# Kernel tuning notes

Measured on AMD Instinct MI355X. Metric: run time of the kernel, lower is better.

The kernel has to match this reference:

```python
import jax, jax.numpy as jnp
import numpy as np

N = 16384
IN_FEATS = 256
OUT_FEATS = 256


def setup_inputs() -> dict:
    key = jax.random.key(0)
    k1, k2, k3, k4 = jax.random.split(key, 4)
    # dense (row-normalized-ish) adjacency; scaled so aggregated values stay O(1)
    graph = jax.random.uniform(k1, (N, N), dtype=jnp.float32) / N
    features = jax.random.normal(k2, (N, IN_FEATS), dtype=jnp.float32)
    # nn.Linear params: W [out, in], b [out]
    W = jax.random.normal(k3, (OUT_FEATS, IN_FEATS), dtype=jnp.float32) / np.sqrt(IN_FEATS)
    b = jax.random.normal(k4, (OUT_FEATS,), dtype=jnp.float32) * 0.01
    return {"graph": graph, "features": features, "W": W, "b": b}


def reference(graph, features, W, b):
    # h = graph @ features  (GCN-style dense neighbor aggregation)
    h = jnp.matmul(graph, features)            # [N, in_feats]
    # linear: h @ W.T + b
    h = jnp.einsum('ni,oi->no', h, W) + b      # [N, out_feats]
    # activation = relu (norm = None)
    return jax.nn.relu(h)
```

## Files before the change

kernel.cpp:

```cpp
#include <hip/hip_runtime.h>
#include <hip/hip_bf16.h>

typedef float f32x4 __attribute__((ext_vector_type(4)));
typedef short short8 __attribute__((ext_vector_type(8)));
typedef __bf16 bf16x8 __attribute__((ext_vector_type(8)));

#define N_TOT 16384
#define FEATS 256
#define BM 128
#define BK 32
#define KSPLIT 4
#define NSTEPS ((N_TOT / KSPLIT) / BK)
#define LDSA_BYTES (BM * 128)
#define LDSB_BYTES (FEATS * 64)
#define TILE_BYTES (LDSA_BYTES + LDSB_BYTES)

static __device__ __forceinline__ ushort f2bf(float f) {
  union { __hip_bfloat16 b; ushort u; } cv;
  cv.b = __float2bfloat16(f);
  return cv.u;
}
static __device__ __forceinline__ float bf2f(ushort u) {
  union { unsigned int i; float f; } c;
  c.i = ((unsigned int)u) << 16;
  return c.f;
}
static __device__ __forceinline__ void gload_lds16(const void* g, void* l) {
  __builtin_amdgcn_global_load_lds((const __attribute__((address_space(1))) unsigned int*)g,
                                   (__attribute__((address_space(3))) unsigned int*)l,
                                   16, 0, 0);
}

__global__ __launch_bounds__(256) void k_transpose(const float* __restrict__ feat,
                                                   ushort* __restrict__ fT) {
  __shared__ float tile[64][65];
  const int tx = threadIdx.x & 63, ty = threadIdx.x >> 6;
  const int k0 = blockIdx.x * 64, n0 = blockIdx.y * 64;
#pragma unroll
  for (int j = 0; j < 64; j += 4)
    tile[ty + j][tx] = feat[(size_t)(k0 + ty + j) * FEATS + n0 + tx];
  __syncthreads();
#pragma unroll
  for (int j = 0; j < 64; j += 4)
    fT[(size_t)(n0 + ty + j) * N_TOT + k0 + tx] = f2bf(tile[tx][ty + j]);
}

__global__ __launch_bounds__(256) void k_convw(const float* __restrict__ W,
                                               ushort* __restrict__ Wb) {
  int i = (blockIdx.x * 256 + threadIdx.x) * 4;
  float4 v = *(const float4*)(W + i);
  ushort4 h = { f2bf(v.x), f2bf(v.y), f2bf(v.z), f2bf(v.w) };
  *(ushort4*)(Wb + i) = h;
}

__global__ __launch_bounds__(512, 4) void k_gemm1(const float* __restrict__ graph,
                                                  const ushort* __restrict__ fT,
                                                  ushort* __restrict__ parts) {
  __shared__ char lds[2][TILE_BYTES];
  const int tid = threadIdx.x;
  const int lane = tid & 63, w = tid >> 6;
  const int wm = w >> 2, wn = w & 3;

  const int b = blockIdx.x;
  const int xcd = b & 7;
  const int kb = xcd >> 1;
  const int mi = (b >> 3) | ((xcd & 1) << 6);
  const size_t m0 = (size_t)mi * BM;
  const int kbase = kb * (N_TOT / KSPLIT);
  const int ph = (b * 53) & (NSTEPS - 1);

  auto stage = [&](int bf, int t) {
    const int k0 = kbase + t * BK;
    char* ldsA = &lds[bf][0];
    char* ldsB = &lds[bf][LDSA_BYTES];
#pragma unroll
    for (int j = 0; j < 2; ++j) {
      const int r0 = w * 16 + j * 8;
      const int row = r0 + (lane >> 3);
      const int c = (lane & 7) ^ (row & 7);
      gload_lds16(graph + (m0 + row) * (size_t)N_TOT + k0 + c * 4, ldsA + r0 * 128);
    }
#pragma unroll
    for (int j = 0; j < 2; ++j) {
      const int r0 = w * 32 + j * 16;
      const int row = r0 + (lane >> 2);
      const int c = (lane & 3) ^ (row & 3);
      gload_lds16(fT + (size_t)row * N_TOT + k0 + c * 8, ldsB + r0 * 64);
    }
  };

  f32x4 acc[4][4] = {};
  const int rsel = lane & 15;
  const int kg = lane >> 4;

  auto compute = [&](int bf) {
    const char* Ab = &lds[bf][0];
    const char* Bb = &lds[bf][LDSA_BYTES];
    short8 bfr[4];
#pragma unroll
    for (int nf = 0; nf < 4; ++nf) {
      const int row = wn * 64 + nf * 16 + rsel;
      const int c = kg ^ (row & 3);
      bfr[nf] = *(const short8*)(Bb + row * 64 + c * 16);
    }
#pragma unroll
    for (int mf = 0; mf < 4; ++mf) {
      const int row = wm * 64 + mf * 16 + rsel;
      const int cb = (row & 7);
      const float4 a0 = *(const float4*)(Ab + row * 128 + ((kg * 2) ^ cb) * 16);
      const float4 a1 = *(const float4*)(Ab + row * 128 + ((kg * 2 + 1) ^ cb) * 16);
      short8 af = { (short)f2bf(a0.x), (short)f2bf(a0.y), (short)f2bf(a0.z), (short)f2bf(a0.w),
                    (short)f2bf(a1.x), (short)f2bf(a1.y), (short)f2bf(a1.z), (short)f2bf(a1.w) };
#pragma unroll
      for (int nf = 0; nf < 4; ++nf)
        acc[mf][nf] = __builtin_amdgcn_mfma_f32_16x16x32_bf16(
            __builtin_bit_cast(bf16x8, af), __builtin_bit_cast(bf16x8, bfr[nf]),
            acc[mf][nf], 0, 0, 0);
    }
  };

  stage(0, ph);
  stage(1, (ph + 1) & (NSTEPS - 1));

  for (int s = 0; s < NSTEPS - 2; ++s) {
    asm volatile("s_waitcnt vmcnt(4)" ::: "memory");
    __builtin_amdgcn_s_barrier();
    __builtin_amdgcn_sched_barrier(0);
    compute(s & 1);
    __builtin_amdgcn_s_barrier();
    stage(s & 1, (s + 2 + ph) & (NSTEPS - 1));
  }
  asm volatile("s_waitcnt vmcnt(4)" ::: "memory");
  __builtin_amdgcn_s_barrier();
  __builtin_amdgcn_sched_barrier(0);
  compute((NSTEPS - 2) & 1);
  asm volatile("s_waitcnt vmcnt(0)" ::: "memory");
  __builtin_amdgcn_s_barrier();
  __builtin_amdgcn_sched_barrier(0);
  compute((NSTEPS - 1) & 1);

  ushort* p = parts + (size_t)kb * N_TOT * FEATS;
#pragma unroll
  for (int mf = 0; mf < 4; ++mf)
#pragma unroll
    for (int nf = 0; nf < 4; ++nf)
#pragma unroll
      for (int j = 0; j < 4; ++j) {
        const int row = wm * 64 + mf * 16 + ((lane >> 4) << 2) + j;
        const int col = wn * 64 + nf * 16 + (lane & 15);
        p[(m0 + row) * FEATS + col] = f2bf(acc[mf][nf][j]);
      }
}

__global__ __launch_bounds__(256) void k_gemm2(const ushort* __restrict__ parts,
                                               const ushort* __restrict__ Wb,
                                               const float* __restrict__ bias,
                                               float* __restrict__ out) {
  __shared__ ushort Al[64][264];
  __shared__ ushort Bl[FEATS][40];
  const int tid = threadIdx.x;
  const int lane = tid & 63, w = tid >> 6;
  const size_t m0 = (size_t)blockIdx.x * 64;

  for (int c = tid; c < 2048; c += 256) {
    const int row = c >> 5;
    const int k8 = (c & 31) << 3;
    const size_t off = (m0 + row) * FEATS + k8;
    float s[8] = {0, 0, 0, 0, 0, 0, 0, 0};
#pragma unroll
    for (int p = 0; p < KSPLIT; ++p) {
      const short8 v = *(const short8*)(parts + (size_t)p * N_TOT * FEATS + off);
#pragma unroll
      for (int j = 0; j < 8; ++j) s[j] += bf2f((ushort)v[j]);
    }
    short8 ov;
#pragma unroll
    for (int j = 0; j < 8; ++j) ov[j] = (short)f2bf(s[j]);
    *(short8*)&Al[row][k8] = ov;
  }

  f32x4 acc[16] = {};
  for (int kk = 0; kk < FEATS; kk += 32) {
    __syncthreads();
#pragma unroll
    for (int q = 0; q < 4; ++q) {
      const short8 v = *(const short8*)(Wb + (size_t)tid * FEATS + kk + q * 8);
      *(short8*)&Bl[tid][q * 8] = v;
    }
    __syncthreads();
    const int koff = (lane >> 4) << 3;
    const short8 af = *(const short8*)&Al[w * 16 + (lane & 15)][kk + koff];
#pragma unroll
    for (int nf = 0; nf < 16; ++nf) {
      const short8 bfv = *(const short8*)&Bl[nf * 16 + (lane & 15)][koff];
      acc[nf] = __builtin_amdgcn_mfma_f32_16x16x32_bf16(
          __builtin_bit_cast(bf16x8, af), __builtin_bit_cast(bf16x8, bfv),
          acc[nf], 0, 0, 0);
    }
  }

#pragma unroll
  for (int nf = 0; nf < 16; ++nf) {
    const int col = nf * 16 + (lane & 15);
    const float bc = bias[col];
#pragma unroll
    for (int j = 0; j < 4; ++j) {
      const int row = w * 16 + ((lane >> 4) << 2) + j;
      const float v = acc[nf][j] + bc;
      out[(m0 + row) * FEATS + col] = fmaxf(v, 0.0f);
    }
  }
}

extern "C" void kernel_launch(void* const* d_in, const int* in_sizes, int n_in,
                              void* d_out, int out_size, void* d_ws, size_t ws_size,
                              hipStream_t stream) {
  const float* graph = (const float*)d_in[0];
  const float* feat  = (const float*)d_in[1];
  const float* W     = (const float*)d_in[2];
  const float* bias  = (const float*)d_in[3];
  float* out = (float*)d_out;

  char* ws = (char*)d_ws;
  ushort* fT    = (ushort*)ws;
  ushort* Wb    = (ushort*)(ws + (size_t)8 * 1024 * 1024);
  ushort* parts = (ushort*)(ws + (size_t)8 * 1024 * 1024 + 131072);

  k_transpose<<<dim3(N_TOT / 64, FEATS / 64), 256, 0, stream>>>(feat, fT);
  k_convw<<<dim3(64), 256, 0, stream>>>(W, Wb);
  k_gemm1<<<dim3((N_TOT / BM) * KSPLIT), 512, 0, stream>>>(graph, fT, parts);
  k_gemm2<<<dim3(N_TOT / 64), 256, 0, stream>>>(parts, Wb, bias, out);
}
```

Measured before the change: 282.7 us.

## Reassociate to graph @ (features @ W^T) and read B operand directly from global

```diff
diff --git a/kernel.cpp b/kernel.cpp
--- a/kernel.cpp
+++ b/kernel.cpp
@@ -8,12 +8,10 @@
 #define N_TOT 16384
 #define FEATS 256
 #define BM 128
-#define BK 32
+#define BK 64
 #define KSPLIT 4
 #define NSTEPS ((N_TOT / KSPLIT) / BK)
-#define LDSA_BYTES (BM * 128)
-#define LDSB_BYTES (FEATS * 64)
-#define TILE_BYTES (LDSA_BYTES + LDSB_BYTES)
+#define LDSA_BYTES (BM * 256)
 
 static __device__ __forceinline__ ushort f2bf(float f) {
   union { __hip_bfloat16 b; ushort u; } cv;
@@ -30,36 +28,50 @@
                                    (__attribute__((address_space(3))) unsigned int*)l,
                                    16, 0, 0);
 }
-
-__global__ __launch_bounds__(256) void k_transpose(const float* __restrict__ feat,
-                                                   ushort* __restrict__ fT) {
-  __shared__ float tile[64][65];
-  const int tx = threadIdx.x & 63, ty = threadIdx.x >> 6;
-  const int k0 = blockIdx.x * 64, n0 = blockIdx.y * 64;
-#pragma unroll
-  for (int j = 0; j < 64; j += 4)
-    tile[ty + j][tx] = feat[(size_t)(k0 + ty + j) * FEATS + n0 + tx];
-  __syncthreads();
-#pragma unroll
-  for (int j = 0; j < 64; j += 4)
-    fT[(size_t)(n0 + ty + j) * N_TOT + k0 + tx] = f2bf(tile[tx][ty + j]);
+static __device__ __forceinline__ bf16x8 cvt8(float4 a, float4 b) {
+  short8 r = { (short)f2bf(a.x), (short)f2bf(a.y), (short)f2bf(a.z), (short)f2bf(a.w),
+               (short)f2bf(b.x), (short)f2bf(b.y), (short)f2bf(b.z), (short)f2bf(b.w) };
+  return __builtin_bit_cast(bf16x8, r);
 }
 
-__global__ __launch_bounds__(256) void k_convw(const float* __restrict__ W,
-                                               ushort* __restrict__ Wb) {
-  int i = (blockIdx.x * 256 + threadIdx.x) * 4;
-  float4 v = *(const float4*)(W + i);
-  ushort4 h = { f2bf(v.x), f2bf(v.y), f2bf(v.z), f2bf(v.w) };
-  *(ushort4*)(Wb + i) = h;
+__global__ __launch_bounds__(64) void k_f2t(const float* __restrict__ feat,
+                                            const float* __restrict__ W,
+                                            ushort* __restrict__ F2T) {
+  const int lane = threadIdx.x;
+  const int rsel = lane & 15, kg = lane >> 4;
+  const int mb = blockIdx.x >> 1;
+  const int o0 = (blockIdx.x & 1) * 128;
+  const int m0 = mb * 16;
+
+  f32x4 acc[8] = {};
+#pragma unroll
+  for (int ks = 0; ks < 8; ++ks) {
+    const int k0 = ks * 32 + kg * 8;
+    const float4 fa0 = *(const float4*)(feat + (size_t)(m0 + rsel) * FEATS + k0);
+    const float4 fa1 = *(const float4*)(feat + (size_t)(m0 + rsel) * FEATS + k0 + 4);
+    const bf16x8 af = cvt8(fa0, fa1);
+#pragma unroll
+    for (int of = 0; of < 8; ++of) {
+      const float4 wb0 = *(const float4*)(W + (size_t)(o0 + of * 16 + rsel) * FEATS + k0);
+      const float4 wb1 = *(const float4*)(W + (size_t)(o0 + of * 16 + rsel) * FEATS + k0 + 4);
+      acc[of] = __builtin_amdgcn_mfma_f32_16x16x32_bf16(af, cvt8(wb0, wb1), acc[of], 0, 0, 0);
+    }
+  }
+#pragma unroll
+  for (int of = 0; of < 8; ++of) {
+    ushort4 ov = { f2bf(acc[of][0]), f2bf(acc[of][1]), f2bf(acc[of][2]), f2bf(acc[of][3]) };
+    *(ushort4*)(F2T + (size_t)(o0 + of * 16 + rsel) * N_TOT + m0 + kg * 4) = ov;
+  }
 }
 
 __global__ __launch_bounds__(512, 4) void k_gemm1(const float* __restrict__ graph,
-                                                  const ushort* __restrict__ fT,
+                                                  const ushort* __restrict__ F2T,
                                                   ushort* __restrict__ parts) {
-  __shared__ char lds[2][TILE_BYTES];
+  __shared__ char lds[2][LDSA_BYTES];
   const int tid = threadIdx.x;
   const int lane = tid & 63, w = tid >> 6;
   const int wm = w >> 2, wn = w & 3;
+  const int rsel = lane & 15, kg = lane >> 4;
 
   const int b = blockIdx.x;
   const int xcd = b & 7;
@@ -67,77 +79,67 @@
   const int mi = (b >> 3) | ((xcd & 1) << 6);
   const size_t m0 = (size_t)mi * BM;
   const int kbase = kb * (N_TOT / KSPLIT);
-  const int ph = (b * 53) & (NSTEPS - 1);
+  const int ph = (b * 29) & (NSTEPS - 1);
 
   auto stage = [&](int bf, int t) {
     const int k0 = kbase + t * BK;
     char* ldsA = &lds[bf][0];
-    char* ldsB = &lds[bf][LDSA_BYTES];
 #pragma unroll
-    for (int j = 0; j < 2; ++j) {
-      const int r0 = w * 16 + j * 8;
-      const int row = r0 + (lane >> 3);
-      const int c = (lane & 7) ^ (row & 7);
-      gload_lds16(graph + (m0 + row) * (size_t)N_TOT + k0 + c * 4, ldsA + r0 * 128);
-    }
-#pragma unroll
-    for (int j = 0; j < 2; ++j) {
-      const int r0 = w * 32 + j * 16;
-      const int row = r0 + (lane >> 2);
-      const int c = (lane & 3) ^ (row & 3);
-      gload_lds16(fT + (size_t)row * N_TOT + k0 + c * 8, ldsB + r0 * 64);
+    for (int j = 0; j < 4; ++j) {
+      const int r0 = j * 32 + w * 4;
+      const int row = r0 + (lane >> 4);
+      const int c = (lane & 15) ^ (row & 15);
+      gload_lds16(graph + (m0 + row) * (size_t)N_TOT + k0 + c * 4, ldsA + r0 * 256);
     }
   };
 
   f32x4 acc[4][4] = {};
-  const int rsel = lane & 15;
-  const int kg = lane >> 4;
 
-  auto compute = [&](int bf) {
+  auto compute = [&](int bf, int t) {
     const char* Ab = &lds[bf][0];
-    const char* Bb = &lds[bf][LDSA_BYTES];
-    short8 bfr[4];
+    const int kglob = kbase + t * BK;
 #pragma unroll
-    for (int nf = 0; nf < 4; ++nf) {
-      const int row = wn * 64 + nf * 16 + rsel;
-      const int c = kg ^ (row & 3);
-      bfr[nf] = *(const short8*)(Bb + row * 64 + c * 16);
-    }
+    for (int ksub = 0; ksub < 2; ++ksub) {
+      short8 bfr[4];
 #pragma unroll
-    for (int mf = 0; mf < 4; ++mf) {
-      const int row = wm * 64 + mf * 16 + rsel;
-      const int cb = (row & 7);
-      const float4 a0 = *(const float4*)(Ab + row * 128 + ((kg * 2) ^ cb) * 16);
-      const float4 a1 = *(const float4*)(Ab + row * 128 + ((kg * 2 + 1) ^ cb) * 16);
-      short8 af = { (short)f2bf(a0.x), (short)f2bf(a0.y), (short)f2bf(a0.z), (short)f2bf(a0.w),
-                    (short)f2bf(a1.x), (short)f2bf(a1.y), (short)f2bf(a1.z), (short)f2bf(a1.w) };
+      for (int nf = 0; nf < 4; ++nf) {
+        const int rowB = wn * 64 + nf * 16 + rsel;
+        bfr[nf] = *(const short8*)(F2T + (size_t)rowB * N_TOT + kglob + ksub * 32 + kg * 8);
+      }
 #pragma unroll
-      for (int nf = 0; nf < 4; ++nf)
-        acc[mf][nf] = __builtin_amdgcn_mfma_f32_16x16x32_bf16(
-            __builtin_bit_cast(bf16x8, af), __builtin_bit_cast(bf16x8, bfr[nf]),
-            acc[mf][nf], 0, 0, 0);
+      for (int mf = 0; mf < 4; ++mf) {
+        const int row = wm * 64 + mf * 16 + rsel;
+        const int cg = ksub * 8 + kg * 2;
+        const float4 a0 = *(const float4*)(Ab + row * 256 + ((cg)     ^ (row & 15)) * 16);
+        const float4 a1 = *(const float4*)(Ab + row * 256 + ((cg + 1) ^ (row & 15)) * 16);
+        const bf16x8 af = cvt8(a0, a1);
+#pragma unroll
+        for (int nf = 0; nf < 4; ++nf)
+          acc[mf][nf] = __builtin_amdgcn_mfma_f32_16x16x32_bf16(
+              af, __builtin_bit_cast(bf16x8, bfr[nf]), acc[mf][nf], 0, 0, 0);
+      }
     }
   };
 
-  stage(0, ph);
-  stage(1, (ph + 1) & (NSTEPS - 1));
+  auto tileof = [&](int s) { return (s + ph) & (NSTEPS - 1); };
+
+  stage(0, tileof(0));
+  stage(1, tileof(1));
 
   for (int s = 0; s < NSTEPS - 2; ++s) {
     asm volatile("s_waitcnt vmcnt(4)" ::: "memory");
     __builtin_amdgcn_s_barrier();
+    compute(s & 1, tileof(s));
+    __builtin_amdgcn_s_barrier();
+    stage(s & 1, tileof(s + 2));
     __builtin_amdgcn_sched_barrier(0);
-    compute(s & 1);
-    __builtin_amdgcn_s_barrier();
-    stage(s & 1, (s + 2 + ph) & (NSTEPS - 1));
   }
   asm volatile("s_waitcnt vmcnt(4)" ::: "memory");
   __builtin_amdgcn_s_barrier();
-  __builtin_amdgcn_sched_barrier(0);
-  compute((NSTEPS - 2) & 1);
+  compute((NSTEPS - 2) & 1, tileof(NSTEPS - 2));
   asm volatile("s_waitcnt vmcnt(0)" ::: "memory");
   __builtin_amdgcn_s_barrier();
-  __builtin_amdgcn_sched_barrier(0);
-  compute((NSTEPS - 1) & 1);
+  compute((NSTEPS - 1) & 1, tileof(NSTEPS - 1));
 
   ushort* p = parts + (size_t)kb * N_TOT * FEATS;
 #pragma unroll
@@ -146,70 +148,32 @@
     for (int nf = 0; nf < 4; ++nf)
 #pragma unroll
       for (int j = 0; j < 4; ++j) {
-        const int row = wm * 64 + mf * 16 + ((lane >> 4) << 2) + j;
-        const int col = wn * 64 + nf * 16 + (lane & 15);
+        const int row = wm * 64 + mf * 16 + kg * 4 + j;
+        const int col = wn * 64 + nf * 16 + rsel;
         p[(m0 + row) * FEATS + col] = f2bf(acc[mf][nf][j]);
       }
 }
 
-__global__ __launch_bounds__(256) void k_gemm2(const ushort* __restrict__ parts,
-                                               const ushort* __restrict__ Wb,
-                                               const float* __restrict__ bias,
-                                               float* __restrict__ out) {
-  __shared__ ushort Al[64][264];
-  __shared__ ushort Bl[FEATS][40];
-  const int tid = threadIdx.x;
-  const int lane = tid & 63, w = tid >> 6;
-  const size_t m0 = (size_t)blockIdx.x * 64;
-
-  for (int c = tid; c < 2048; c += 256) {
-    const int row = c >> 5;
-    const int k8 = (c & 31) << 3;
-    const size_t off = (m0 + row) * FEATS + k8;
-    float s[8] = {0, 0, 0, 0, 0, 0, 0, 0};
+__global__ __launch_bounds__(256) void k_reduce(const ushort* __restrict__ parts,
+                                                const float* __restrict__ bias,
+                                                float* __restrict__ out) {
+  const size_t base = ((size_t)blockIdx.x * 256 + threadIdx.x) * 8;
+  const int o0 = (int)(base & (FEATS - 1));
+  float s[8] = {0, 0, 0, 0, 0, 0, 0, 0};
 #pragma unroll
-    for (int p = 0; p < KSPLIT; ++p) {
-      const short8 v = *(const short8*)(parts + (size_t)p * N_TOT * FEATS + off);
+  for (int p = 0; p < KSPLIT; ++p) {
+    const short8 v = *(const short8*)(parts + (size_t)p * N_TOT * FEATS + base);
 #pragma unroll
-      for (int j = 0; j < 8; ++j) s[j] += bf2f((ushort)v[j]);
-    }
-    short8 ov;
-#pragma unroll
-    for (int j = 0; j < 8; ++j) ov[j] = (short)f2bf(s[j]);
-    *(short8*)&Al[row][k8] = ov;
+    for (int j = 0; j < 8; ++j) s[j] += bf2f((ushort)v[j]);
   }
-
-  f32x4 acc[16] = {};
-  for (int kk = 0; kk < FEATS; kk += 32) {
-    __syncthreads();
-#pragma unroll
-    for (int q = 0; q < 4; ++q) {
-      const short8 v = *(const short8*)(Wb + (size_t)tid * FEATS + kk + q * 8);
-      *(short8*)&Bl[tid][q * 8] = v;
-    }
-    __syncthreads();
-    const int koff = (lane >> 4) << 3;
-    const short8 af = *(const short8*)&Al[w * 16 + (lane & 15)][kk + koff];
-#pragma unroll
-    for (int nf = 0; nf < 16; ++nf) {
-      const short8 bfv = *(const short8*)&Bl[nf * 16 + (lane & 15)][koff];
-      acc[nf] = __builtin_amdgcn_mfma_f32_16x16x32_bf16(
-          __builtin_bit_cast(bf16x8, af), __builtin_bit_cast(bf16x8, bfv),
-          acc[nf], 0, 0, 0);
-    }
-  }
-
-#pragma unroll
-  for (int nf = 0; nf < 16; ++nf) {
-    const int col = nf * 16 + (lane & 15);
-    const float bc = bias[col];
-#pragma unroll
-    for (int j = 0; j < 4; ++j) {
-      const int row = w * 16 + ((lane >> 4) << 2) + j;
-      const float v = acc[nf][j] + bc;
-      out[(m0 + row) * FEATS + col] = fmaxf(v, 0.0f);
-    }
-  }
+  const float4 b0 = *(const float4*)(bias + o0);
+  const float4 b1 = *(const float4*)(bias + o0 + 4);
+  float4 r0 = { fmaxf(s[0] + b0.x, 0.f), fmaxf(s[1] + b0.y, 0.f),
+                fmaxf(s[2] + b0.z, 0.f), fmaxf(s[3] + b0.w, 0.f) };
+  float4 r1 = { fmaxf(s[4] + b1.x, 0.f), fmaxf(s[5] + b1.y, 0.f),
+                fmaxf(s[6] + b1.z, 0.f), fmaxf(s[7] + b1.w, 0.f) };
+  *(float4*)(out + base) = r0;
+  *(float4*)(out + base + 4) = r1;
 }
 
 extern "C" void kernel_launch(void* const* d_in, const int* in_sizes, int n_in,
@@ -222,12 +186,10 @@
   float* out = (float*)d_out;
 
   char* ws = (char*)d_ws;
-  ushort* fT    = (ushort*)ws;
-  ushort* Wb    = (ushort*)(ws + (size_t)8 * 1024 * 1024);
-  ushort* parts = (ushort*)(ws + (size_t)8 * 1024 * 1024 + 131072);
+  ushort* F2T   = (ushort*)ws;
+  ushort* parts = (ushort*)(ws + (size_t)8 * 1024 * 1024);
 
-  k_transpose<<<dim3(N_TOT / 64, FEATS / 64), 256, 0, stream>>>(feat, fT);
-  k_convw<<<dim3(64), 256, 0, stream>>>(W, Wb);
-  k_gemm1<<<dim3((N_TOT / BM) * KSPLIT), 512, 0, stream>>>(graph, fT, parts);
-  k_gemm2<<<dim3(N_TOT / 64), 256, 0, stream>>>(parts, Wb, bias, out);
+  k_f2t<<<dim3(2048), 64, 0, stream>>>(feat, W, F2T);
+  k_gemm1<<<dim3((N_TOT / BM) * KSPLIT), 512, 0, stream>>>(graph, F2T, parts);
+  k_reduce<<<dim3(N_TOT * FEATS / 8 / 256), 256, 0, stream>>>(parts, bias, out);
 }
```

After: 396.4 us. 1.4x slower.

## Stage graph tile through registers, converting to bf16 once before LDS

Applied to the files above, without the earlier changes.

```diff
diff --git a/kernel.cpp b/kernel.cpp
--- a/kernel.cpp
+++ b/kernel.cpp
@@ -11,9 +11,9 @@
 #define BK 32
 #define KSPLIT 4
 #define NSTEPS ((N_TOT / KSPLIT) / BK)
-#define LDSA_BYTES (BM * 128)
-#define LDSB_BYTES (FEATS * 64)
-#define TILE_BYTES (LDSA_BYTES + LDSB_BYTES)
+#define LDSA_B (BM * 64)
+#define LDSB_B (FEATS * 64)
+#define TILE_B (LDSA_B + LDSB_B)
 
 static __device__ __forceinline__ ushort f2bf(float f) {
   union { __hip_bfloat16 b; ushort u; } cv;
@@ -56,61 +56,59 @@
 __global__ __launch_bounds__(512, 4) void k_gemm1(const float* __restrict__ graph,
                                                   const ushort* __restrict__ fT,
                                                   ushort* __restrict__ parts) {
-  __shared__ char lds[2][TILE_BYTES];
-  const int tid = threadIdx.x;
-  const int lane = tid & 63, w = tid >> 6;
+  __shared__ char lds[2][TILE_B];
+  const int tid = threadIdx.x, lane = tid & 63, w = tid >> 6;
   const int wm = w >> 2, wn = w & 3;
-
-  const int b = blockIdx.x;
-  const int xcd = b & 7;
-  const int kb = xcd >> 1;
+  const int rsel = lane & 15, kg = lane >> 4;
+
+  const int b = blockIdx.x, xcd = b & 7, kb = xcd >> 1;
   const int mi = (b >> 3) | ((xcd & 1) << 6);
   const size_t m0 = (size_t)mi * BM;
   const int kbase = kb * (N_TOT / KSPLIT);
   const int ph = (b * 53) & (NSTEPS - 1);
 
-  auto stage = [&](int bf, int t) {
+  const int arow = tid >> 2;
+  const int acol = tid & 3;
+  const int aslot = acol ^ ((arow >> 1) & 3);
+  const float* asrc = graph + (m0 + arow) * (size_t)N_TOT + kbase + acol * 8;
+
+  auto issueA = [&](float4 (&r)[2], int t) {
+    const float* p = asrc + t * BK;
+    r[0] = *(const float4*)(p);
+    r[1] = *(const float4*)(p + 4);
+  };
+  auto writeA = [&](int bf, const float4 (&r)[2]) {
+    short8 h = { (short)f2bf(r[0].x), (short)f2bf(r[0].y), (short)f2bf(r[0].z), (short)f2bf(r[0].w),
+                 (short)f2bf(r[1].x), (short)f2bf(r[1].y), (short)f2bf(r[1].z), (short)f2bf(r[1].w) };
+    *(short8*)(&lds[bf][arow * 64 + aslot * 16]) = h;
+  };
+  auto issueB = [&](int bf, int t) {
     const int k0 = kbase + t * BK;
-    char* ldsA = &lds[bf][0];
-    char* ldsB = &lds[bf][LDSA_BYTES];
-#pragma unroll
-    for (int j = 0; j < 2; ++j) {
-      const int r0 = w * 16 + j * 8;
-      const int row = r0 + (lane >> 3);
-      const int c = (lane & 7) ^ (row & 7);
-      gload_lds16(graph + (m0 + row) * (size_t)N_TOT + k0 + c * 4, ldsA + r0 * 128);
-    }
+    char* ldsB = &lds[bf][LDSA_B];
 #pragma unroll
     for (int j = 0; j < 2; ++j) {
       const int r0 = w * 32 + j * 16;
       const int row = r0 + (lane >> 2);
-      const int c = (lane & 3) ^ (row & 3);
+      const int c = (lane & 3) ^ ((row >> 1) & 3);
       gload_lds16(fT + (size_t)row * N_TOT + k0 + c * 8, ldsB + r0 * 64);
     }
   };
 
   f32x4 acc[4][4] = {};
-  const int rsel = lane & 15;
-  const int kg = lane >> 4;
 
   auto compute = [&](int bf) {
     const char* Ab = &lds[bf][0];
-    const char* Bb = &lds[bf][LDSA_BYTES];
+    const char* Bb = &lds[bf][LDSA_B];
     short8 bfr[4];
 #pragma unroll
     for (int nf = 0; nf < 4; ++nf) {
       const int row = wn * 64 + nf * 16 + rsel;
-      const int c = kg ^ (row & 3);
-      bfr[nf] = *(const short8*)(Bb + row * 64 + c * 16);
+      bfr[nf] = *(const short8*)(Bb + row * 64 + (kg ^ ((row >> 1) & 3)) * 16);
     }
 #pragma unroll
     for (int mf = 0; mf < 4; ++mf) {
       const int row = wm * 64 + mf * 16 + rsel;
-      const int cb = (row & 7);
-      const float4 a0 = *(const float4*)(Ab + row * 128 + ((kg * 2) ^ cb) * 16);
-      const float4 a1 = *(const float4*)(Ab + row * 128 + ((kg * 2 + 1) ^ cb) * 16);
-      short8 af = { (short)f2bf(a0.x), (short)f2bf(a0.y), (short)f2bf(a0.z), (short)f2bf(a0.w),
-                    (short)f2bf(a1.x), (short)f2bf(a1.y), (short)f2bf(a1.z), (short)f2bf(a1.w) };
+      const short8 af = *(const short8*)(Ab + row * 64 + (kg ^ ((row >> 1) & 3)) * 16);
 #pragma unroll
       for (int nf = 0; nf < 4; ++nf)
         acc[mf][nf] = __builtin_amdgcn_mfma_f32_16x16x32_bf16(
@@ -119,25 +117,41 @@
     }
   };
 
-  stage(0, ph);
-  stage(1, (ph + 1) & (NSTEPS - 1));
-
-  for (int s = 0; s < NSTEPS - 2; ++s) {
-    asm volatile("s_waitcnt vmcnt(4)" ::: "memory");
-    __builtin_amdgcn_s_barrier();
-    __builtin_amdgcn_sched_barrier(0);
-    compute(s & 1);
-    __builtin_amdgcn_s_barrier();
-    stage(s & 1, (s + 2 + ph) & (NSTEPS - 1));
-  }
+  auto tileof = [&](int s) { return (s + ph) & (NSTEPS - 1); };
+  float4 rA0[2], rA1[2];
+
+  issueA(rA0, tileof(0));
+  issueB(0, tileof(0));
+  issueA(rA1, tileof(1));
+  issueB(1, tileof(1));
   asm volatile("s_waitcnt vmcnt(4)" ::: "memory");
+  writeA(0, rA0);
+  asm volatile("s_waitcnt lgkmcnt(0)" ::: "memory");
+  __builtin_amdgcn_sched_barrier(0);
   __builtin_amdgcn_s_barrier();
-  __builtin_amdgcn_sched_barrier(0);
-  compute((NSTEPS - 2) & 1);
-  asm volatile("s_waitcnt vmcnt(0)" ::: "memory");
-  __builtin_amdgcn_s_barrier();
-  __builtin_amdgcn_sched_barrier(0);
-  compute((NSTEPS - 1) & 1);
+
+  for (int s = 0; s < NSTEPS; s += 2) {
+    issueA(rA0, tileof(s + 2));
+    __builtin_amdgcn_sched_barrier(0);
+    compute(0);
+    __builtin_amdgcn_s_barrier();
+    asm volatile("s_waitcnt vmcnt(2)" ::: "memory");
+    writeA(1, rA1);
+    issueB(0, tileof(s + 2));
+    asm volatile("s_waitcnt lgkmcnt(0)" ::: "memory");
+    __builtin_amdgcn_sched_barrier(0);
+    __builtin_amdgcn_s_barrier();
+    issueA(rA1, tileof(s + 3));
+    __builtin_amdgcn_sched_barrier(0);
+    compute(1);
+    __builtin_amdgcn_s_barrier();
+    asm volatile("s_waitcnt vmcnt(2)" ::: "memory");
+    writeA(0, rA0);
+    issueB(1, tileof(s + 3));
+    asm volatile("s_waitcnt lgkmcnt(0)" ::: "memory");
+    __builtin_amdgcn_sched_barrier(0);
+    __builtin_amdgcn_s_barrier();
+  }
 
   ushort* p = parts + (size_t)kb * N_TOT * FEATS;
 #pragma unroll
@@ -146,8 +160,8 @@
     for (int nf = 0; nf < 4; ++nf)
 #pragma unroll
       for (int j = 0; j < 4; ++j) {
-        const int row = wm * 64 + mf * 16 + ((lane >> 4) << 2) + j;
-        const int col = wn * 64 + nf * 16 + (lane & 15);
+        const int row = wm * 64 + mf * 16 + kg * 4 + j;
+        const int col = wn * 64 + nf * 16 + rsel;
         p[(m0 + row) * FEATS + col] = f2bf(acc[mf][nf][j]);
       }
 }
```

New measurement: 299.2 us. +5.8%, slower.
